# Performance work log

Hardware: AMD Instinct MI355X
Metric: run time of the kernel (lower is better)

Reference implementation:

```python
import jax, jax.numpy as jnp
import numpy as np


def setup_inputs() -> dict:
    key = jax.random.key(0)
    k1, k2, k3, k4 = jax.random.split(key, 4)
    N, E, D, B = 50000, 100000, 64, 16
    atom_features = jax.random.normal(k1, (N, D), dtype=jnp.float32)
    bond_features = jax.random.normal(k2, (E, B), dtype=jnp.float32)
    pair_indices = jax.random.randint(k3, (E, 2), 0, N, dtype=jnp.int32)
    kernel = jax.random.normal(k4, (B, D * D), dtype=jnp.float32) * (1.0 / np.sqrt(B))
    bias = jnp.zeros((D * D,), dtype=jnp.float32)
    return {
        "atom_features": atom_features,
        "bond_features": bond_features,
        "pair_indices": pair_indices,
        "kernel": kernel,
        "bias": bias,
    }


def reference(atom_features, bond_features, pair_indices, kernel, bias):
    N, D = atom_features.shape
    # Per-edge transformation matrix: [E, D, D]
    edge_mat = (bond_features @ kernel + bias).reshape(-1, D, D)
    # Gather neighbor atom features: [E, D]
    neighbors = atom_features[pair_indices[:, 1]]
    # Per-edge matvec (matmul with expand/squeeze in original): [E, D]
    transformed = jnp.einsum("eij,ej->ei", edge_mat, neighbors)
    # Scatter-add into destination atoms: [N, D]
    aggregated = jax.ops.segment_sum(transformed, pair_indices[:, 0], num_segments=N)
    return aggregated
```

## Files before the change

### kernel.cpp

```cpp
#include <hip/hip_runtime.h>

typedef _Float16 half8  __attribute__((ext_vector_type(8)));
typedef _Float16 half2v __attribute__((ext_vector_type(2)));
typedef float    f32x4  __attribute__((ext_vector_type(4)));

#define BB 16
#define KB 17
#define BM 128
#define PACK_BLKS 34
#define ZERO_BLKS 2048

__global__ void prep(const float* __restrict__ kern, const float* __restrict__ bias,
                     _Float16* __restrict__ ktg, f32x4* __restrict__ out4, int n4) {
  if (blockIdx.x < PACK_BLKS) {
    int g = blockIdx.x * 256 + threadIdx.x;
    int s = g >> 8, t = (g >> 6) & 3, l = g & 63;
    int i = t * 16 + (l & 15);
    int k0 = s * 32 + (l >> 4) * 8;
    _Float16 v[8];
#pragma unroll
    for (int e = 0; e < 8; ++e) {
      int k = k0 + e, b = k >> 6, j = k & 63;
      float x = (b < BB) ? kern[b * 4096 + i * 64 + j] : bias[i * 64 + j];
      v[e] = (_Float16)x;
    }
    *(half8*)(ktg + (size_t)g * 8) = *(const half8*)v;
  } else {
    int i = (blockIdx.x - PACK_BLKS) * 256 + threadIdx.x;
    for (; i < n4; i += ZERO_BLKS * 256) out4[i] = (f32x4){0.f, 0.f, 0.f, 0.f};
  }
}

__device__ __forceinline__ uint32_t dup16(float x) {
  union { half2v h; uint32_t u; } c;
  _Float16 hv = (_Float16)x;
  c.h = (half2v){hv, hv};
  return c.u;
}

__global__ __launch_bounds__(512, 6)
void edge_gemm(const float* __restrict__ atom, const float* __restrict__ bond,
               const int* __restrict__ pair, const _Float16* __restrict__ ktg,
               float* __restrict__ out, int E) {
  __shared__ __align__(16) char smem[32768];
  __shared__ uint32_t bnd2[BM * KB];
  __shared__ int srcs[BM];

  const int tid = threadIdx.x;
  const int e0  = blockIdx.x * BM;

  {
    const int r = tid >> 2, q = tid & 3;
    const int e = e0 + r;
    const bool valid = e < E;
    const int nbr = valid ? pair[2 * e + 1] : 0;

    f32x4 bv = {0.f, 0.f, 0.f, 0.f};
    if (valid) bv = ((const f32x4*)(bond + (size_t)e * BB))[q];
#pragma unroll
    for (int z = 0; z < 4; ++z) bnd2[r * KB + q * 4 + z] = dup16(bv[z]);
    if (q == 3) bnd2[r * KB + 16] = dup16(valid ? 1.0f : 0.0f);
    if (q == 2) srcs[r] = valid ? pair[2 * e] : 0;

    const f32x4* arow = (const f32x4*)(atom + (size_t)nbr * 64);
#pragma unroll
    for (int cc = 0; cc < 2; ++cc) {
      const int c8 = q * 2 + cc;
      f32x4 x0 = {0.f,0.f,0.f,0.f}, x1 = {0.f,0.f,0.f,0.f};
      if (valid) { x0 = arow[2 * c8]; x1 = arow[2 * c8 + 1]; }
      _Float16 h[8];
      h[0] = (_Float16)x0[0]; h[1] = (_Float16)x0[1]; h[2] = (_Float16)x0[2]; h[3] = (_Float16)x0[3];
      h[4] = (_Float16)x1[0]; h[5] = (_Float16)x1[1]; h[6] = (_Float16)x1[2]; h[7] = (_Float16)x1[3];
      *(half8*)(smem + r * 128 + ((c8 ^ (r & 7)) << 4)) = *(const half8*)h;
    }
  }
  __syncthreads();

  const int lane = tid & 63, wave = tid >> 6;
  const int kh = wave & 1, mg = wave >> 1;
  const int l15 = lane & 15, lg = lane >> 4;
  const int R0 = mg * 32 + l15, R1 = R0 + 16;
  const int rb0 = R0 * 128, rb1 = R1 * 128;
  const int sw  = (l15 & 7) << 4;
  const char* nbb = smem;
  const _Float16* bp = ktg + (size_t)(kh * 17) * 2048 + (size_t)lane * 8;
  const int khb = kh * 8;

  f32x4 acc[2][4];
#pragma unroll
  for (int t = 0; t < 2; ++t)
#pragma unroll
    for (int n = 0; n < 4; ++n) acc[t][n] = (f32x4){0.f, 0.f, 0.f, 0.f};

#define STEP(p_, i_, j_) do {                                                   \
    const int c16 = (((p_) * 4 + lg) << 4) ^ sw;                                \
    half8 a0 = *(const half8*)(nbb + rb0 + c16);                                \
    half8 a1 = *(const half8*)(nbb + rb1 + c16);                                \
    union { uint32_t u; half2v h; } s0, s1;                                     \
    s0.u = bnd2[R0 * KB + khb + (i_)];                                          \
    s1.u = bnd2[R1 * KB + khb + (i_)];                                          \
    half2v* a0p = (half2v*)&a0; half2v* a1p = (half2v*)&a1;                     \
    _Pragma("unroll") for (int qq = 0; qq < 4; ++qq) {                          \
      a0p[qq] = a0p[qq] * s0.h; a1p[qq] = a1p[qq] * s1.h; }                     \
    _Pragma("unroll") for (int nt = 0; nt < 4; ++nt) {                          \
      const half8 bf = *(const half8*)(bp + (j_) * 2048 + nt * 512);            \
      acc[0][nt] = __builtin_amdgcn_mfma_f32_16x16x32_f16(a0, bf, acc[0][nt], 0, 0, 0); \
      acc[1][nt] = __builtin_amdgcn_mfma_f32_16x16x32_f16(a1, bf, acc[1][nt], 0, 0, 0); \
    } } while (0)

  if (kh == 0) {
#pragma unroll
    for (int j = 0; j < 17; ++j) STEP(j & 1, j >> 1, j);
  } else {
#pragma unroll
    for (int j = 0; j < 17; ++j) STEP((j + 1) & 1, (j + 1) >> 1, j);
  }
#undef STEP

  __syncthreads();

  char* red = smem;
  if (kh == 1) {
#pragma unroll
    for (int t = 0; t < 2; ++t)
#pragma unroll
      for (int n = 0; n < 4; ++n) {
        const int i8 = t * 4 + n;
        *(f32x4*)(red + mg * 8192 + lane * 128 + ((i8 ^ (lane & 7)) << 4)) = acc[t][n];
      }
  }
  __syncthreads();
  if (kh == 0) {
#pragma unroll
    for (int t = 0; t < 2; ++t)
#pragma unroll
      for (int n = 0; n < 4; ++n) {
        const int i8 = t * 4 + n;
        f32x4 o = *(const f32x4*)(red + mg * 8192 + lane * 128 + ((i8 ^ (lane & 7)) << 4));
        acc[t][n] += o;
      }
#pragma unroll
    for (int t = 0; t < 2; ++t) {
#pragma unroll
      for (int rr = 0; rr < 4; ++rr) {
        const int el = mg * 32 + t * 16 + lg * 4 + rr;
        if (e0 + el < E) {
          float* dst = out + (size_t)srcs[el] * 64 + l15;
          atomicAdd(dst,      acc[t][0][rr]);
          atomicAdd(dst + 16, acc[t][1][rr]);
          atomicAdd(dst + 32, acc[t][2][rr]);
          atomicAdd(dst + 48, acc[t][3][rr]);
        }
      }
    }
  }
}

extern "C" void kernel_launch(void* const* d_in, const int* in_sizes, int n_in,
                              void* d_out, int out_size, void* d_ws, size_t ws_size,
                              hipStream_t stream) {
  const float* atom = (const float*)d_in[0];
  const float* bond = (const float*)d_in[1];
  const int*   pair = (const int*)d_in[2];
  const float* kern = (const float*)d_in[3];
  const float* bias = (const float*)d_in[4];
  float* out = (float*)d_out;
  _Float16* ktg = (_Float16*)d_ws;

  const int E  = in_sizes[1] / BB;
  const int n4 = out_size / 4;

  prep<<<PACK_BLKS + ZERO_BLKS, 256, 0, stream>>>(kern, bias, ktg, (f32x4*)out, n4);
  edge_gemm<<<(E + BM - 1) / BM, 512, 0, stream>>>(atom, bond, pair, ktg, out, E);
}
```

Measured before the change: 127.8 us.

## Restructure edge GEMM: waves split output columns, stage kernel slices via LDS double-buffer

The edge GEMM block drops from 512 to 256 threads. Each wave now owns 16 output columns for all 128 edges instead of splitting the K dimension, which removes the cross-wave LDS reduction. Kernel-weight slices are loaded into a double-buffered LDS tile with global_load_lds, overlapping the next slice's load with the current MFMAs, and the packed weight layout is reordered so each slice is contiguous. The cost is a __syncthreads per K-slice, more A fragments held in registers per wave (NT=8), and lower thread count per block.

```diff
diff --git a/kernel.cpp b/kernel.cpp
--- a/kernel.cpp
+++ b/kernel.cpp
@@ -5,10 +5,17 @@
 typedef float    f32x4  __attribute__((ext_vector_type(4)));
 
 #define BB 16
-#define KB 17
+#define NB_B 17
 #define BM 128
+#define NT 8
 #define PACK_BLKS 34
-#define ZERO_BLKS 2048
+#define ZERO_BLKS 1024
+
+__device__ __forceinline__ void gll16(const void* g, void* l) {
+  __builtin_amdgcn_global_load_lds(
+      (const __attribute__((address_space(1))) void*)g,
+      (__attribute__((address_space(3))) void*)l, 16, 0, 0);
+}
 
 __global__ void prep(const float* __restrict__ kern, const float* __restrict__ bias,
                      _Float16* __restrict__ ktg, f32x4* __restrict__ out4, int n4) {
@@ -24,134 +31,122 @@
       float x = (b < BB) ? kern[b * 4096 + i * 64 + j] : bias[i * 64 + j];
       v[e] = (_Float16)x;
     }
-    *(half8*)(ktg + (size_t)g * 8) = *(const half8*)v;
+    size_t dst = (size_t)(s >> 1) * 4096 + (size_t)(s & 1) * 2048 + t * 512 + l * 8;
+    *(half8*)(ktg + dst) = *(const half8*)v;
   } else {
     int i = (blockIdx.x - PACK_BLKS) * 256 + threadIdx.x;
     for (; i < n4; i += ZERO_BLKS * 256) out4[i] = (f32x4){0.f, 0.f, 0.f, 0.f};
   }
 }
 
-__device__ __forceinline__ uint32_t dup16(float x) {
-  union { half2v h; uint32_t u; } c;
-  _Float16 hv = (_Float16)x;
-  c.h = (half2v){hv, hv};
-  return c.u;
-}
-
-__global__ __launch_bounds__(512, 6)
+__global__ __launch_bounds__(256, 4)
 void edge_gemm(const float* __restrict__ atom, const float* __restrict__ bond,
                const int* __restrict__ pair, const _Float16* __restrict__ ktg,
                float* __restrict__ out, int E) {
-  __shared__ __align__(16) char smem[32768];
-  __shared__ uint32_t bnd2[BM * KB];
+  __shared__ __align__(16) _Float16 nb[BM * 64];
+  __shared__ __align__(16) char bbuf[2][8192];
+  __shared__ __align__(16) _Float16 bndh[NB_B * 16 * NT];
   __shared__ int srcs[BM];
+  __shared__ int nbrs[BM];
 
   const int tid = threadIdx.x;
   const int e0  = blockIdx.x * BM;
 
-  {
-    const int r = tid >> 2, q = tid & 3;
-    const int e = e0 + r;
+  if (tid < BM) {
+    const int e = e0 + tid;
     const bool valid = e < E;
-    const int nbr = valid ? pair[2 * e + 1] : 0;
+    int2 p2 = valid ? *(const int2*)(pair + 2 * e) : (int2){0, 0};
+    srcs[tid] = p2.x;
+    nbrs[tid] = p2.y;
+  }
+  gll16((const char*)ktg + tid * 16,        (char*)bbuf[0] + tid * 16);
+  gll16((const char*)ktg + 4096 + tid * 16, (char*)bbuf[0] + 4096 + tid * 16);
+  __syncthreads();
 
-    f32x4 bv = {0.f, 0.f, 0.f, 0.f};
-    if (valid) bv = ((const f32x4*)(bond + (size_t)e * BB))[q];
+  if (tid < BM) {
+    const int e = e0 + tid;
+    const bool valid = e < E;
+    const int wl = tid & 15, wt = tid >> 4;
+    const f32x4* brow = (const f32x4*)(bond + (size_t)e * BB);
 #pragma unroll
-    for (int z = 0; z < 4; ++z) bnd2[r * KB + q * 4 + z] = dup16(bv[z]);
-    if (q == 3) bnd2[r * KB + 16] = dup16(valid ? 1.0f : 0.0f);
-    if (q == 2) srcs[r] = valid ? pair[2 * e] : 0;
+    for (int q = 0; q < 4; ++q) {
+      f32x4 bv = {0.f, 0.f, 0.f, 0.f};
+      if (valid) bv = brow[q];
+#pragma unroll
+      for (int z = 0; z < 4; ++z)
+        bndh[((q * 4 + z) * 16 + wl) * NT + wt] = (_Float16)bv[z];
+    }
+    bndh[(16 * 16 + wl) * NT + wt] = valid ? (_Float16)1.0f : (_Float16)0.0f;
+  }
 
-    const f32x4* arow = (const f32x4*)(atom + (size_t)nbr * 64);
 #pragma unroll
-    for (int cc = 0; cc < 2; ++cc) {
-      const int c8 = q * 2 + cc;
-      f32x4 x0 = {0.f,0.f,0.f,0.f}, x1 = {0.f,0.f,0.f,0.f};
-      if (valid) { x0 = arow[2 * c8]; x1 = arow[2 * c8 + 1]; }
-      _Float16 h[8];
-      h[0] = (_Float16)x0[0]; h[1] = (_Float16)x0[1]; h[2] = (_Float16)x0[2]; h[3] = (_Float16)x0[3];
-      h[4] = (_Float16)x1[0]; h[5] = (_Float16)x1[1]; h[6] = (_Float16)x1[2]; h[7] = (_Float16)x1[3];
-      *(half8*)(smem + r * 128 + ((c8 ^ (r & 7)) << 4)) = *(const half8*)h;
+  for (int it = 0; it < 4; ++it) {
+    const int idx = it * 256 + tid;
+    const int r = idx >> 3, c8 = idx & 7;
+    const int nbr = nbrs[r];
+    const bool valid = (e0 + r) < E;
+    f32x4 x0 = {0.f,0.f,0.f,0.f}, x1 = {0.f,0.f,0.f,0.f};
+    if (valid) {
+      const f32x4* arow = (const f32x4*)(atom + (size_t)nbr * 64);
+      x0 = arow[2 * c8]; x1 = arow[2 * c8 + 1];
     }
+    _Float16 h[8];
+    h[0] = (_Float16)x0[0]; h[1] = (_Float16)x0[1]; h[2] = (_Float16)x0[2]; h[3] = (_Float16)x0[3];
+    h[4] = (_Float16)x1[0]; h[5] = (_Float16)x1[1]; h[6] = (_Float16)x1[2]; h[7] = (_Float16)x1[3];
+    *(half8*)((char*)nb + r * 128 + ((c8 ^ (r & 7)) << 4)) = *(const half8*)h;
   }
   __syncthreads();
 
   const int lane = tid & 63, wave = tid >> 6;
-  const int kh = wave & 1, mg = wave >> 1;
   const int l15 = lane & 15, lg = lane >> 4;
-  const int R0 = mg * 32 + l15, R1 = R0 + 16;
-  const int rb0 = R0 * 128, rb1 = R1 * 128;
-  const int sw  = (l15 & 7) << 4;
-  const char* nbb = smem;
-  const _Float16* bp = ktg + (size_t)(kh * 17) * 2048 + (size_t)lane * 8;
-  const int khb = kh * 8;
 
-  f32x4 acc[2][4];
+  half8 a[NT][2];
 #pragma unroll
-  for (int t = 0; t < 2; ++t)
+  for (int t = 0; t < NT; ++t) {
+    const int r = t * 16 + l15;
+    const int rb = r * 128, sw = (r & 7) << 4;
 #pragma unroll
-    for (int n = 0; n < 4; ++n) acc[t][n] = (f32x4){0.f, 0.f, 0.f, 0.f};
+    for (int p = 0; p < 2; ++p)
+      a[t][p] = *(const half8*)((const char*)nb + rb + (((p * 4 + lg) << 4) ^ sw));
+  }
 
-#define STEP(p_, i_, j_) do {                                                   \
-    const int c16 = (((p_) * 4 + lg) << 4) ^ sw;                                \
-    half8 a0 = *(const half8*)(nbb + rb0 + c16);                                \
-    half8 a1 = *(const half8*)(nbb + rb1 + c16);                                \
-    union { uint32_t u; half2v h; } s0, s1;                                     \
-    s0.u = bnd2[R0 * KB + khb + (i_)];                                          \
-    s1.u = bnd2[R1 * KB + khb + (i_)];                                          \
-    half2v* a0p = (half2v*)&a0; half2v* a1p = (half2v*)&a1;                     \
-    _Pragma("unroll") for (int qq = 0; qq < 4; ++qq) {                          \
-      a0p[qq] = a0p[qq] * s0.h; a1p[qq] = a1p[qq] * s1.h; }                     \
-    _Pragma("unroll") for (int nt = 0; nt < 4; ++nt) {                          \
-      const half8 bf = *(const half8*)(bp + (j_) * 2048 + nt * 512);            \
-      acc[0][nt] = __builtin_amdgcn_mfma_f32_16x16x32_f16(a0, bf, acc[0][nt], 0, 0, 0); \
-      acc[1][nt] = __builtin_amdgcn_mfma_f32_16x16x32_f16(a1, bf, acc[1][nt], 0, 0, 0); \
-    } } while (0)
+  f32x4 acc[NT];
+#pragma unroll
+  for (int t = 0; t < NT; ++t) acc[t] = (f32x4){0.f, 0.f, 0.f, 0.f};
 
-  if (kh == 0) {
+  for (int b = 0; b < NB_B; ++b) {
+    if (b + 1 < NB_B) {
+      const char* src = (const char*)ktg + (size_t)(b + 1) * 8192;
+      char* dst = (char*)bbuf[(b + 1) & 1];
+      gll16(src + tid * 16,        dst + tid * 16);
+      gll16(src + 4096 + tid * 16, dst + 4096 + tid * 16);
+    }
+    const half8 sv = *(const half8*)&bndh[(b * 16 + l15) * NT];
+    const char* bp = (const char*)bbuf[b & 1] + wave * 1024 + lane * 16;
 #pragma unroll
-    for (int j = 0; j < 17; ++j) STEP(j & 1, j >> 1, j);
-  } else {
+    for (int sp = 0; sp < 2; ++sp) {
+      const half8 bf = *(const half8*)(bp + sp * 4096);
 #pragma unroll
-    for (int j = 0; j < 17; ++j) STEP((j + 1) & 1, (j + 1) >> 1, j);
+      for (int t = 0; t < NT; ++t) {
+        const _Float16 s = sv[t];
+        const half2v sc = {s, s};
+        half8 as = a[t][sp];
+        half2v* ap = (half2v*)&as;
+#pragma unroll
+        for (int q = 0; q < 4; ++q) ap[q] = ap[q] * sc;
+        acc[t] = __builtin_amdgcn_mfma_f32_16x16x32_f16(as, bf, acc[t], 0, 0, 0);
+      }
+    }
+    __syncthreads();
   }
-#undef STEP
 
-  __syncthreads();
-
-  char* red = smem;
-  if (kh == 1) {
 #pragma unroll
-    for (int t = 0; t < 2; ++t)
+  for (int t = 0; t < NT; ++t) {
 #pragma unroll
-      for (int n = 0; n < 4; ++n) {
-        const int i8 = t * 4 + n;
-        *(f32x4*)(red + mg * 8192 + lane * 128 + ((i8 ^ (lane & 7)) << 4)) = acc[t][n];
-      }
-  }
-  __syncthreads();
-  if (kh == 0) {
-#pragma unroll
-    for (int t = 0; t < 2; ++t)
-#pragma unroll
-      for (int n = 0; n < 4; ++n) {
-        const int i8 = t * 4 + n;
-        f32x4 o = *(const f32x4*)(red + mg * 8192 + lane * 128 + ((i8 ^ (lane & 7)) << 4));
-        acc[t][n] += o;
-      }
-#pragma unroll
-    for (int t = 0; t < 2; ++t) {
-#pragma unroll
-      for (int rr = 0; rr < 4; ++rr) {
-        const int el = mg * 32 + t * 16 + lg * 4 + rr;
-        if (e0 + el < E) {
-          float* dst = out + (size_t)srcs[el] * 64 + l15;
-          atomicAdd(dst,      acc[t][0][rr]);
-          atomicAdd(dst + 16, acc[t][1][rr]);
-          atomicAdd(dst + 32, acc[t][2][rr]);
-          atomicAdd(dst + 48, acc[t][3][rr]);
-        }
-      }
+    for (int rr = 0; rr < 4; ++rr) {
+      const int el = t * 16 + lg * 4 + rr;
+      if (e0 + el < E)
+        atomicAdd(out + (size_t)srcs[el] * 64 + wave * 16 + l15, acc[t][rr]);
     }
   }
 }
@@ -171,5 +166,5 @@
   const int n4 = out_size / 4;
 
   prep<<<PACK_BLKS + ZERO_BLKS, 256, 0, stream>>>(kern, bias, ktg, (f32x4*)out, n4);
-  edge_gemm<<<(E + BM - 1) / BM, 512, 0, stream>>>(atom, bond, pair, ktg, out, E);
+  edge_gemm<<<(E + BM - 1) / BM, 256, 0, stream>>>(atom, bond, pair, ktg, out, E);
 }
```

Result: faster. 115.1 us (-10.0%).
